# Kernel optimization log

Hardware: AMD Instinct MI355X
Metric: run time of the kernel (lower is better)

Reference implementation:

```python
import jax, jax.numpy as jnp
import numpy as np

N = 16384
E = 262144
HID = 128
NFILT = 128
NGAUSS = 50
NINTER = 6
CUTOFF = 10.0
NUMZ = 100
LOG2 = 0.6931471805599453


def ssp(x):
    # ShiftedSoftplus
    return jax.nn.softplus(x) - LOG2


def setup_inputs() -> dict:
    key = jax.random.key(0)
    ks = jax.random.split(key, 20)
    z = jax.random.randint(ks[0], (N,), 0, NUMZ)
    pos = jax.random.uniform(ks[1], (N, 3), dtype=jnp.float32) * 5.0  # box side 5 -> all pairs < cutoff
    edge_index = jax.random.randint(ks[2], (2, E), 0, N)
    s = lambda k, shape, fan: jax.random.normal(k, shape, dtype=jnp.float32) / np.sqrt(fan)
    params = dict(
        emb=s(ks[3], (NUMZ, HID), 1.0),
        Wf1=s(ks[4], (NINTER, NGAUSS, NFILT), NGAUSS), bf1=jnp.zeros((NINTER, NFILT), jnp.float32),
        Wf2=s(ks[5], (NINTER, NFILT, NFILT), NFILT), bf2=jnp.zeros((NINTER, NFILT), jnp.float32),
        Wl1=s(ks[6], (NINTER, HID, NFILT), HID),
        Wl2=s(ks[7], (NINTER, NFILT, HID), NFILT), bl2=jnp.zeros((NINTER, HID), jnp.float32),
        Wl=s(ks[8], (NINTER, HID, HID), HID), bl=jnp.zeros((NINTER, HID), jnp.float32),
        Wo1=s(ks[9], (HID, HID // 2), HID), bo1=jnp.zeros((HID // 2,), jnp.float32),
        Wo2=s(ks[10], (HID // 2, 1), HID // 2), bo2=jnp.zeros((1,), jnp.float32),
    )
    return dict(z=z, pos=pos, edge_index=edge_index, **params)


def reference(z, pos, edge_index, emb, Wf1, bf1, Wf2, bf2, Wl1, Wl2, bl2, Wl, bl, Wo1, bo1, Wo2, bo2):
    src, dst = edge_index[0], edge_index[1]
    # edge distances and Gaussian smearing
    d = jnp.linalg.norm(pos[src] - pos[dst], axis=-1)          # [E]
    offset = jnp.linspace(0.0, CUTOFF, NGAUSS, dtype=jnp.float32)
    coeff = -0.5 / (offset[1] - offset[0]) ** 2
    ea = jnp.exp(coeff * (d[:, None] - offset) ** 2)            # [E, NGAUSS]
    C = 0.5 * (jnp.cos(d * (np.pi / CUTOFF)) + 1.0)             # cosine cutoff [E]

    h = emb[z]                                                  # [N, HID]
    for i in range(NINTER):
        # continuous-filter weights
        Wfilt = (ssp(ea @ Wf1[i] + bf1[i]) @ Wf2[i] + bf2[i]) * C[:, None]  # [E, NFILT]
        x = h @ Wl1[i]                                          # lin1, no bias [N, NFILT]
        msg = x[src] * Wfilt                                    # gather + filter
        agg = jax.ops.segment_sum(msg, dst, num_segments=N)     # scatter-sum [N, NFILT]
        x = ssp(agg @ Wl2[i] + bl2[i]) @ Wl[i] + bl[i]          # lin2 -> ssp -> lin
        h = h + x

    h = ssp(h @ Wo1 + bo1) @ Wo2 + bo2                          # [N, 1] per-atom energy
    out = jnp.sum(h, axis=0, keepdims=True)                     # 'add' readout, single graph -> [1, 1]
    return jax.nn.relu(out)
```

## Files before the change

kernel.cpp:

```cpp
#include <hip/hip_runtime.h>
#include <math.h>

#define NATOM 16384
#define NEDGE 262144
#define HID 128
#define NG 50
#define NI 6

typedef _Float16 h8_t __attribute__((ext_vector_type(8)));
typedef _Float16 h4_t __attribute__((ext_vector_type(4)));
typedef float    f4_t __attribute__((ext_vector_type(4)));

__device__ __forceinline__ float ssp_f(float v) {
    float e = __expf(-fabsf(v));
    return fmaxf(v, 0.0f) + __logf(1.0f + e) - 0.69314718055994531f;
}

__global__ void fill0(float* __restrict__ p, int n4) {
    int i = blockIdx.x * 256 + threadIdx.x;
    if (i < n4) ((float4*)p)[i] = make_float4(0.f, 0.f, 0.f, 0.f);
}

__global__ void hist_k(const int* __restrict__ ei, int* __restrict__ cnt) {
    int e = blockIdx.x * 256 + threadIdx.x;
    if (e < NEDGE) atomicAdd(&cnt[ei[NEDGE + e]], 1);
}

__global__ void scan_k(const int* __restrict__ cnt, int* __restrict__ offs) {
    __shared__ int part[256];
    int t = threadIdx.x;
    int base = t * 64;
    int s = 0;
    for (int i = 0; i < 64; ++i) s += cnt[base + i];
    part[t] = s;
    __syncthreads();
    for (int off = 1; off < 256; off <<= 1) {
        int v = (t >= off) ? part[t - off] : 0;
        __syncthreads();
        part[t] += v;
        __syncthreads();
    }
    int r = part[t] - s;
    for (int i = 0; i < 64; ++i) { offs[base + i] = r; r += cnt[base + i]; }
    if (t == 255) offs[NATOM] = r;
}

__global__ void scatter_k(const int* __restrict__ ei, const int* __restrict__ offs,
                          int* __restrict__ cnt, int* __restrict__ sSrc, int* __restrict__ sDst) {
    int e = blockIdx.x * 256 + threadIdx.x;
    if (e >= NEDGE) return;
    int d = ei[NEDGE + e];
    int r = atomicAdd(&cnt[d], 1);
    int j = offs[d] + r;
    sSrc[j] = ei[e];
    sDst[j] = d;
}

__global__ void edge_pre(const float* __restrict__ pos,
                         const int* __restrict__ sSrc, const int* __restrict__ sDst,
                         _Float16* __restrict__ ea, float* __restrict__ Cb) {
    int j = blockIdx.x * 256 + threadIdx.x;
    if (j >= NEDGE) return;
    int s = sSrc[j], dd = sDst[j];
    float dx = pos[3*s]   - pos[3*dd];
    float dy = pos[3*s+1] - pos[3*dd+1];
    float dz = pos[3*s+2] - pos[3*dd+2];
    float d = sqrtf(dx*dx + dy*dy + dz*dz);
    Cb[j] = 0.5f * (cosf(d * 0.31415926535897931f) + 1.0f);
    const float delta = 10.0f / 49.0f;
    const float coeff = -0.5f / (delta * delta);
    #pragma unroll
    for (int gq = 0; gq < 8; ++gq) {
        h8_t hv;
        #pragma unroll
        for (int r = 0; r < 8; ++r) {
            int g = gq * 8 + r;
            float v = 0.0f;
            if (g < NG) { float u = d - (float)g * delta; v = __expf(coeff * u * u); }
            hv[r] = (_Float16)v;
        }
        *(h8_t*)&ea[(size_t)j * 64 + gq * 8] = hv;
    }
}

__global__ void wprep(const float* __restrict__ Wf1, const float* __restrict__ Wf2,
                      const float* __restrict__ Wl1, const float* __restrict__ Wl2,
                      const float* __restrict__ Wl,
                      _Float16* __restrict__ w1, _Float16* __restrict__ w2,
                      _Float16* __restrict__ wnh, _Float16* __restrict__ wnl) {
    int idx = blockIdx.x * 256 + threadIdx.x;
    const int S1 = NI * 128 * 64, S2 = NI * 128 * 128;
    if (idx < S1) {
        int i = idx >> 13, r = idx & 8191, fo = r >> 6, k = r & 63;
        float v = (k < NG) ? Wf1[(size_t)i * NG * 128 + k * 128 + fo] : 0.0f;
        w1[idx] = (_Float16)v;
        return;
    }
    idx -= S1;
    if (idx < S2) {
        int i = idx >> 14, r = idx & 16383, fo = r >> 7, k = r & 127;
        w2[idx] = (_Float16)Wf2[(size_t)i * 128 * 128 + k * 128 + fo];
        return;
    }
    idx -= S2;
    if (idx < 3 * S2) {
        int mi = idx >> 14;
        int r = idx & 16383, fo = r >> 7, k = r & 127;
        int m = mi / NI, i = mi % NI;
        const float* W = (m == 0) ? Wl1 : (m == 1) ? Wl2 : Wl;
        float v = W[(size_t)i * 128 * 128 + k * 128 + fo];
        _Float16 hh = (_Float16)v;
        wnh[idx] = hh; wnl[idx] = (_Float16)(v - (float)hh);
    }
}

__global__ void embed_k(const int* __restrict__ z, const float* __restrict__ emb,
                        float* __restrict__ h) {
    int tid = blockIdx.x * 256 + threadIdx.x;
    int n = tid >> 7, f = tid & 127;
    h[tid] = emb[z[n] * HID + f];
}

__launch_bounds__(256)
__global__ void gemm_node_mfma(const float* __restrict__ A,
                               const _Float16* __restrict__ wth, const _Float16* __restrict__ wtl,
                               _Float16* __restrict__ xh) {
    __shared__ _Float16 aH[64 * 136];
    __shared__ _Float16 aL[64 * 136];
    int t = threadIdx.x;
    int mb = blockIdx.x * 64;
    #pragma unroll
    for (int j = 0; j < 8; ++j) {
        int idx = t + j * 256;
        int row = idx >> 5, c4 = idx & 31;
        f4_t v = *(const f4_t*)&A[(size_t)(mb + row) * HID + c4 * 4];
        h4_t hh, ll;
        #pragma unroll
        for (int r = 0; r < 4; ++r) {
            _Float16 hx = (_Float16)v[r];
            hh[r] = hx; ll[r] = (_Float16)(v[r] - (float)hx);
        }
        *(h4_t*)&aH[row * 136 + c4 * 4] = hh;
        *(h4_t*)&aL[row * 136 + c4 * 4] = ll;
    }
    __syncthreads();

    int wv = t >> 6, lane = t & 63, l15 = lane & 15, quad = lane >> 4;
    f4_t acc[2][4];
    #pragma unroll
    for (int m = 0; m < 2; ++m)
        #pragma unroll
        for (int n = 0; n < 4; ++n) acc[m][n] = (f4_t)0.0f;

    for (int kc = 0; kc < 4; ++kc) {
        int k0 = kc * 32 + quad * 8;
        h8_t a_h[2], a_l[2];
        #pragma unroll
        for (int m = 0; m < 2; ++m) {
            int fr = wv * 32 + m * 16 + l15;
            a_h[m] = *(const h8_t*)&wth[fr * 128 + k0];
            a_l[m] = *(const h8_t*)&wtl[fr * 128 + k0];
        }
        #pragma unroll
        for (int n = 0; n < 4; ++n) {
            int er = n * 16 + l15;
            h8_t b_h = *(const h8_t*)&aH[er * 136 + k0];
            h8_t b_l = *(const h8_t*)&aL[er * 136 + k0];
            #pragma unroll
            for (int m = 0; m < 2; ++m) {
                acc[m][n] = __builtin_amdgcn_mfma_f32_16x16x32_f16(a_h[m], b_h, acc[m][n], 0, 0, 0);
                acc[m][n] = __builtin_amdgcn_mfma_f32_16x16x32_f16(a_h[m], b_l, acc[m][n], 0, 0, 0);
                acc[m][n] = __builtin_amdgcn_mfma_f32_16x16x32_f16(a_l[m], b_h, acc[m][n], 0, 0, 0);
            }
        }
    }

    #pragma unroll
    for (int n = 0; n < 4; ++n) {
        int el = n * 16 + l15;
        size_t row = (size_t)(mb + el);
        #pragma unroll
        for (int m = 0; m < 2; ++m) {
            int fb = wv * 32 + m * 16 + quad * 4;
            h4_t o;
            #pragma unroll
            for (int r = 0; r < 4; ++r) o[r] = (_Float16)acc[m][n][r];
            *(h4_t*)&xh[row * 128 + fb] = o;
        }
    }
}

__launch_bounds__(256)
__global__ void gemm_node3(const float* __restrict__ agg,
                           const _Float16* __restrict__ w2th, const _Float16* __restrict__ w2tl,
                           const _Float16* __restrict__ wlth, const _Float16* __restrict__ wltl,
                           const _Float16* __restrict__ w1nh, const _Float16* __restrict__ w1nl,
                           const float* __restrict__ bl2, const float* __restrict__ bl,
                           float* __restrict__ h, _Float16* __restrict__ xh) {
    __shared__ _Float16 aH[64 * 136];
    __shared__ _Float16 aL[64 * 136];
    int t = threadIdx.x;
    int mb = blockIdx.x * 64;
    #pragma unroll
    for (int j = 0; j < 8; ++j) {
        int idx = t + j * 256;
        int row = idx >> 5, c4 = idx & 31;
        f4_t v = *(const f4_t*)&agg[(size_t)(mb + row) * HID + c4 * 4];
        h4_t hh, ll;
        #pragma unroll
        for (int r = 0; r < 4; ++r) {
            _Float16 hx = (_Float16)v[r];
            hh[r] = hx; ll[r] = (_Float16)(v[r] - (float)hx);
        }
        *(h4_t*)&aH[row * 136 + c4 * 4] = hh;
        *(h4_t*)&aL[row * 136 + c4 * 4] = ll;
    }
    __syncthreads();

    int wv = t >> 6, lane = t & 63, l15 = lane & 15, quad = lane >> 4;
    int fq = wv * 32 + quad * 4;
    f4_t acc[2][4];

    #pragma unroll
    for (int m = 0; m < 2; ++m)
        #pragma unroll
        for (int n = 0; n < 4; ++n) acc[m][n] = (f4_t)0.0f;
    for (int kc = 0; kc < 4; ++kc) {
        int k0 = kc * 32 + quad * 8;
        h8_t a_h[2], a_l[2];
        #pragma unroll
        for (int m = 0; m < 2; ++m) {
            int fr = wv * 32 + m * 16 + l15;
            a_h[m] = *(const h8_t*)&w2th[fr * 128 + k0];
            a_l[m] = *(const h8_t*)&w2tl[fr * 128 + k0];
        }
        #pragma unroll
        for (int n = 0; n < 4; ++n) {
            int er = n * 16 + l15;
            h8_t b_h = *(const h8_t*)&aH[er * 136 + k0];
            h8_t b_l = *(const h8_t*)&aL[er * 136 + k0];
            #pragma unroll
            for (int m = 0; m < 2; ++m) {
                acc[m][n] = __builtin_amdgcn_mfma_f32_16x16x32_f16(a_h[m], b_h, acc[m][n], 0, 0, 0);
                acc[m][n] = __builtin_amdgcn_mfma_f32_16x16x32_f16(a_h[m], b_l, acc[m][n], 0, 0, 0);
                acc[m][n] = __builtin_amdgcn_mfma_f32_16x16x32_f16(a_l[m], b_h, acc[m][n], 0, 0, 0);
            }
        }
    }
    f4_t b2v[2];
    b2v[0] = *(const f4_t*)&bl2[fq]; b2v[1] = *(const f4_t*)&bl2[fq + 16];
    __syncthreads();

    #pragma unroll
    for (int m = 0; m < 2; ++m)
        #pragma unroll
        for (int n = 0; n < 4; ++n) {
            int el = n * 16 + l15;
            int fb = wv * 32 + m * 16 + quad * 4;
            h4_t hh, ll;
            #pragma unroll
            for (int r = 0; r < 4; ++r) {
                float sv = ssp_f(acc[m][n][r] + b2v[m][r]);
                _Float16 hx = (_Float16)sv;
                hh[r] = hx;
                ll[r] = (_Float16)(sv - (float)hx);
            }
            *(h4_t*)&aH[el * 136 + fb] = hh;
            *(h4_t*)&aL[el * 136 + fb] = ll;
        }
    __syncthreads();

    #pragma unroll
    for (int m = 0; m < 2; ++m)
        #pragma unroll
        for (int n = 0; n < 4; ++n) acc[m][n] = (f4_t)0.0f;
    for (int kc = 0; kc < 4; ++kc) {
        int k0 = kc * 32 + quad * 8;
        h8_t a_h[2], a_l[2];
        #pragma unroll
        for (int m = 0; m < 2; ++m) {
            int fr = wv * 32 + m * 16 + l15;
            a_h[m] = *(const h8_t*)&wlth[fr * 128 + k0];
            a_l[m] = *(const h8_t*)&wltl[fr * 128 + k0];
        }
        #pragma unroll
        for (int n = 0; n < 4; ++n) {
            int er = n * 16 + l15;
            h8_t b_h = *(const h8_t*)&aH[er * 136 + k0];
            h8_t b_l = *(const h8_t*)&aL[er * 136 + k0];
            #pragma unroll
            for (int m = 0; m < 2; ++m) {
                acc[m][n] = __builtin_amdgcn_mfma_f32_16x16x32_f16(a_h[m], b_h, acc[m][n], 0, 0, 0);
                acc[m][n] = __builtin_amdgcn_mfma_f32_16x16x32_f16(a_h[m], b_l, acc[m][n], 0, 0, 0);
                acc[m][n] = __builtin_amdgcn_mfma_f32_16x16x32_f16(a_l[m], b_h, acc[m][n], 0, 0, 0);
            }
        }
    }
    f4_t blv[2];
    blv[0] = *(const f4_t*)&bl[fq]; blv[1] = *(const f4_t*)&bl[fq + 16];
    __syncthreads();

    #pragma unroll
    for (int n = 0; n < 4; ++n) {
        int el = n * 16 + l15;
        size_t row = (size_t)(mb + el);
        #pragma unroll
        for (int m = 0; m < 2; ++m) {
            int fb = wv * 32 + m * 16 + quad * 4;
            f4_t hv = *(const f4_t*)&h[row * 128 + fb];
            f4_t o;
            h4_t hh, ll;
            #pragma unroll
            for (int r = 0; r < 4; ++r) {
                o[r] = hv[r] + acc[m][n][r] + blv[m][r];
                _Float16 hx = (_Float16)o[r];
                hh[r] = hx; ll[r] = (_Float16)(o[r] - (float)hx);
            }
            *(f4_t*)&h[row * 128 + fb] = o;
            *(h4_t*)&aH[el * 136 + fb] = hh;
            *(h4_t*)&aL[el * 136 + fb] = ll;
        }
    }
    if (!w1nh) return;
    __syncthreads();

    #pragma unroll
    for (int m = 0; m < 2; ++m)
        #pragma unroll
        for (int n = 0; n < 4; ++n) acc[m][n] = (f4_t)0.0f;
    for (int kc = 0; kc < 4; ++kc) {
        int k0 = kc * 32 + quad * 8;
        h8_t a_h[2], a_l[2];
        #pragma unroll
        for (int m = 0; m < 2; ++m) {
            int fr = wv * 32 + m * 16 + l15;
            a_h[m] = *(const h8_t*)&w1nh[fr * 128 + k0];
            a_l[m] = *(const h8_t*)&w1nl[fr * 128 + k0];
        }
        #pragma unroll
        for (int n = 0; n < 4; ++n) {
            int er = n * 16 + l15;
            h8_t b_h = *(const h8_t*)&aH[er * 136 + k0];
            h8_t b_l = *(const h8_t*)&aL[er * 136 + k0];
            #pragma unroll
            for (int m = 0; m < 2; ++m) {
                acc[m][n] = __builtin_amdgcn_mfma_f32_16x16x32_f16(a_h[m], b_h, acc[m][n], 0, 0, 0);
                acc[m][n] = __builtin_amdgcn_mfma_f32_16x16x32_f16(a_h[m], b_l, acc[m][n], 0, 0, 0);
                acc[m][n] = __builtin_amdgcn_mfma_f32_16x16x32_f16(a_l[m], b_h, acc[m][n], 0, 0, 0);
            }
        }
    }
    #pragma unroll
    for (int n = 0; n < 4; ++n) {
        int el = n * 16 + l15;
        size_t row = (size_t)(mb + el);
        #pragma unroll
        for (int m = 0; m < 2; ++m) {
            int fb = wv * 32 + m * 16 + quad * 4;
            h4_t o;
            #pragma unroll
            for (int r = 0; r < 4; ++r) o[r] = (_Float16)acc[m][n][r];
            *(h4_t*)&xh[row * 128 + fb] = o;
        }
    }
}

#define T1_LDW 136
#define EA_LDW 72
#define EF_TPB 4

__launch_bounds__(256, 4)
__global__ void edge_filter(const _Float16* __restrict__ xh, float* __restrict__ agg,
                            const int* __restrict__ sSrc, const int* __restrict__ sDst,
                            const float* __restrict__ Cb,
                            const _Float16* __restrict__ ea,
                            const _Float16* __restrict__ w1, const _Float16* __restrict__ w2,
                            const float* __restrict__ bf1, const float* __restrict__ bf2) {
    __shared__ __align__(16) _Float16 eaS[64 * EA_LDW];
    __shared__ __align__(16) _Float16 t1S[64 * T1_LDW];
    __shared__ int dstl[64];

    _Float16* msg = t1S;

    int t = threadIdx.x;
    int wv = t >> 6, lane = t & 63;
    int l15 = lane & 15, quad = lane >> 4;
    int tile0 = blockIdx.x * EF_TPB;

    h8_t w1f[2][2], w2f[4][2];
    #pragma unroll
    for (int kc = 0; kc < 2; ++kc) {
        int k0 = kc * 32 + quad * 8;
        #pragma unroll
        for (int m = 0; m < 2; ++m)
            w1f[kc][m] = *(const h8_t*)&w1[(wv * 32 + m * 16 + l15) * 64 + k0];
    }
    #pragma unroll
    for (int kc = 0; kc < 4; ++kc) {
        int k0 = kc * 32 + quad * 8;
        #pragma unroll
        for (int m = 0; m < 2; ++m)
            w2f[kc][m] = *(const h8_t*)&w2[(wv * 32 + m * 16 + l15) * 128 + k0];
    }
    int fq = wv * 32 + quad * 4;
    f4_t b1v[2], b2v[2];
    b1v[0] = *(const f4_t*)&bf1[fq];  b1v[1] = *(const f4_t*)&bf1[fq + 16];
    b2v[0] = *(const f4_t*)&bf2[fq];  b2v[1] = *(const f4_t*)&bf2[fq + 16];

    int srcn[4], dstn[4];
    float cn[4];
    {
        int eb = tile0 * 64;
        #pragma unroll
        for (int n = 0; n < 4; ++n) {
            int ge = eb + n * 16 + l15;
            srcn[n] = sSrc[ge];
            dstn[n] = sDst[ge];
            cn[n]   = Cb[ge];
        }
        if (t < 64) dstl[t] = sDst[eb + t];
        #pragma unroll
        for (int c = 0; c < 2; ++c) {
            int ch = t + c * 256;
            int e = ch >> 3, ks = ch & 7;
            *(h8_t*)&eaS[e * EA_LDW + ks * 8] = *(const h8_t*)&ea[(size_t)(eb + e) * 64 + ks * 8];
        }
    }
    __syncthreads();

    for (int tt = 0; tt < EF_TPB; ++tt) {
        bool pre = (tt < EF_TPB - 1);
        h8_t sreg[2];
        int srcp[4], dstp[4];
        float cp[4];
        if (pre) {
            int ebn = (tile0 + tt + 1) * 64;
            #pragma unroll
            for (int c = 0; c < 2; ++c) {
                int ch = t + c * 256;
                int e = ch >> 3, ks = ch & 7;
                sreg[c] = *(const h8_t*)&ea[(size_t)(ebn + e) * 64 + ks * 8];
            }
            #pragma unroll
            for (int n = 0; n < 4; ++n) {
                int ge = ebn + n * 16 + l15;
                srcp[n] = sSrc[ge];
                dstp[n] = sDst[ge];
                cp[n]   = Cb[ge];
            }
        }
        h4_t xr[4][2];
        #pragma unroll
        for (int n = 0; n < 4; ++n)
            #pragma unroll
            for (int m = 0; m < 2; ++m)
                xr[n][m] = *(const h4_t*)&xh[(size_t)srcn[n] * HID + wv * 32 + m * 16 + quad * 4];

        f4_t acc1[2][4];
        #pragma unroll
        for (int m = 0; m < 2; ++m)
            #pragma unroll
            for (int n = 0; n < 4; ++n) acc1[m][n] = (f4_t)0.0f;
        #pragma unroll
        for (int kc = 0; kc < 2; ++kc) {
            int k0 = kc * 32 + quad * 8;
            h8_t b[4];
            #pragma unroll
            for (int n = 0; n < 4; ++n)
                b[n] = *(const h8_t*)&eaS[(n * 16 + l15) * EA_LDW + k0];
            #pragma unroll
            for (int m = 0; m < 2; ++m)
                #pragma unroll
                for (int n = 0; n < 4; ++n)
                    acc1[m][n] = __builtin_amdgcn_mfma_f32_16x16x32_f16(w1f[kc][m], b[n], acc1[m][n], 0, 0, 0);
        }

        #pragma unroll
        for (int m = 0; m < 2; ++m)
            #pragma unroll
            for (int n = 0; n < 4; ++n) {
                int el = n * 16 + l15;
                int fb = wv * 32 + m * 16 + quad * 4;
                h4_t hh;
                #pragma unroll
                for (int r = 0; r < 4; ++r)
                    hh[r] = (_Float16)ssp_f(acc1[m][n][r] + b1v[m][r]);
                *(h4_t*)&t1S[el * T1_LDW + fb] = hh;
            }
        __syncthreads();

        if (pre) {
            #pragma unroll
            for (int c = 0; c < 2; ++c) {
                int ch = t + c * 256;
                int e = ch >> 3, ks = ch & 7;
                *(h8_t*)&eaS[e * EA_LDW + ks * 8] = sreg[c];
            }
        }

        f4_t acc2[2][4];
        #pragma unroll
        for (int m = 0; m < 2; ++m)
            #pragma unroll
            for (int n = 0; n < 4; ++n) acc2[m][n] = (f4_t)0.0f;
        #pragma unroll
        for (int kc = 0; kc < 4; ++kc) {
            int k0 = kc * 32 + quad * 8;
            #pragma unroll
            for (int n = 0; n < 4; ++n) {
                h8_t b = *(const h8_t*)&t1S[(n * 16 + l15) * T1_LDW + k0];
                #pragma unroll
                for (int m = 0; m < 2; ++m)
                    acc2[m][n] = __builtin_amdgcn_mfma_f32_16x16x32_f16(w2f[kc][m], b, acc2[m][n], 0, 0, 0);
            }
        }
        __syncthreads();

        #pragma unroll
        for (int n = 0; n < 4; ++n) {
            int el = n * 16 + l15;
            float ce = cn[n];
            #pragma unroll
            for (int m = 0; m < 2; ++m) {
                int fb = wv * 32 + m * 16 + quad * 4;
                h4_t o;
                #pragma unroll
                for (int r = 0; r < 4; ++r)
                    o[r] = (_Float16)((acc2[m][n][r] + b2v[m][r]) * ce * (float)xr[n][m][r]);
                *(h4_t*)&msg[el * T1_LDW + fb] = o;
            }
        }
        __syncthreads();

        {
            int f = t & 127, hf = t >> 7;
            int ib = hf * 32;
            float run = 0.0f;
            int cur = dstl[ib];
            for (int i = ib; i < ib + 32; ++i) {
                int dnow = dstl[i];
                if (dnow != cur) {
                    atomicAdd(&agg[(size_t)cur * HID + f], run);
                    run = 0.0f;
                    cur = dnow;
                }
                run += (float)msg[i * T1_LDW + f];
            }
            atomicAdd(&agg[(size_t)cur * HID + f], run);
        }

        if (pre) {
            #pragma unroll
            for (int n = 0; n < 4; ++n) { srcn[n] = srcp[n]; dstn[n] = dstp[n]; cn[n] = cp[n]; }
            __syncthreads();
            if (t < 64) dstl[t] = dstp[t >> 4] ;
        }
    }
}

__launch_bounds__(256)
__global__ void readout1(const float* __restrict__ h, const float* __restrict__ Wo1,
                         const float* __restrict__ bo1, const float* __restrict__ Wo2,
                         const float* __restrict__ bo2, float* __restrict__ accum) {
    __shared__ float w1[128 * 64];
    __shared__ float part[4];
    int t = threadIdx.x;
    for (int i = t; i < 128 * 16; i += 256)
        ((float4*)w1)[i] = ((const float4*)Wo1)[i];
    __syncthreads();
    int f = t & 63, wv = t >> 6;
    float b = bo1[f], w2v = Wo2[f];
    float lsum = 0.0f;
    for (int a = 0; a < 16; ++a) {
        int n = blockIdx.x * 64 + wv * 16 + a;
        const float* hr = &h[(size_t)n * HID];
        float acc = b;
        #pragma unroll 16
        for (int k = 0; k < 128; ++k)
            acc = fmaf(hr[k], w1[k*64 + f], acc);
        lsum += ssp_f(acc) * w2v;
    }
    #pragma unroll
    for (int off = 32; off > 0; off >>= 1)
        lsum += __shfl_down(lsum, off, 64);
    if (f == 0) part[wv] = lsum;
    __syncthreads();
    if (t == 0)
        atomicAdd(accum, part[0] + part[1] + part[2] + part[3] + 64.0f * bo2[0]);
}

__global__ void readout2(const float* __restrict__ accum, float* __restrict__ out) {
    out[0] = fmaxf(accum[0], 0.0f);
}

extern "C" void kernel_launch(void* const* d_in, const int* in_sizes, int n_in,
                              void* d_out, int out_size, void* d_ws, size_t ws_size,
                              hipStream_t stream) {
    const int*   z   = (const int*)d_in[0];
    const float* pos = (const float*)d_in[1];
    const int*   ei  = (const int*)d_in[2];
    const float* emb = (const float*)d_in[3];
    const float* Wf1 = (const float*)d_in[4];
    const float* bf1 = (const float*)d_in[5];
    const float* Wf2 = (const float*)d_in[6];
    const float* bf2 = (const float*)d_in[7];
    const float* Wl1 = (const float*)d_in[8];
    const float* Wl2 = (const float*)d_in[9];
    const float* bl2 = (const float*)d_in[10];
    const float* Wl  = (const float*)d_in[11];
    const float* bl  = (const float*)d_in[12];
    const float* Wo1 = (const float*)d_in[13];
    const float* bo1 = (const float*)d_in[14];
    const float* Wo2 = (const float*)d_in[15];
    const float* bo2 = (const float*)d_in[16];
    float* out = (float*)d_out;

    _Float16* w1  = (_Float16*)d_ws;
    _Float16* w2  = w1 + NI * 8192;
    _Float16* wnh = w2 + NI * 16384;
    _Float16* wnl = wnh + 3 * NI * 16384;
    _Float16* ea  = wnl + 3 * NI * 16384;
    _Float16* xh  = ea + (size_t)NEDGE * 64;
    float* Cb  = (float*)(xh + (size_t)NATOM * 128);
    float* h   = Cb + NEDGE;
    float* agg = h + (size_t)NATOM * HID;
    float* accum = agg + (size_t)NATOM * HID;
    int* cnt  = (int*)(accum + 4);
    int* offs = cnt + NATOM;
    int* sSrc = offs + NATOM + 4;
    int* sDst = sSrc + NEDGE;

    fill0<<<NATOM/4/256, 256, 0, stream>>>((float*)cnt, NATOM/4);
    hist_k<<<NEDGE/256, 256, 0, stream>>>(ei, cnt);
    scan_k<<<1, 256, 0, stream>>>(cnt, offs);
    fill0<<<NATOM/4/256, 256, 0, stream>>>((float*)cnt, NATOM/4);
    scatter_k<<<NEDGE/256, 256, 0, stream>>>(ei, offs, cnt, sSrc, sDst);

    edge_pre<<<NEDGE/256, 256, 0, stream>>>(pos, sSrc, sDst, ea, Cb);
    wprep<<<(NI*8192 + NI*16384 + 3*NI*16384)/256, 256, 0, stream>>>(
        Wf1, Wf2, Wl1, Wl2, Wl, w1, w2, wnh, wnl);
    embed_k<<<(NATOM*HID)/256, 256, 0, stream>>>(z, emb, h);

    gemm_node_mfma<<<256, 256, 0, stream>>>(h, wnh + (size_t)0*16384,
        wnl + (size_t)0*16384, xh);
    for (int i = 0; i < NI; ++i) {
        fill0<<<(NATOM*HID/4)/256, 256, 0, stream>>>(agg, NATOM*HID/4);
        edge_filter<<<NEDGE/64/EF_TPB, 256, 0, stream>>>(xh, agg, sSrc, sDst, Cb, ea,
            w1 + (size_t)i*8192, w2 + (size_t)i*16384,
            bf1 + i*HID, bf2 + i*HID);
        const _Float16* w1nh = (i < NI-1) ? wnh + (size_t)(i+1)*16384 : nullptr;
        const _Float16* w1nl = (i < NI-1) ? wnl + (size_t)(i+1)*16384 : nullptr;
        gemm_node3<<<256, 256, 0, stream>>>(agg,
            wnh + (size_t)(1*NI+i)*16384, wnl + (size_t)(1*NI+i)*16384,
            wnh + (size_t)(2*NI+i)*16384, wnl + (size_t)(2*NI+i)*16384,
            w1nh, w1nl, bl2 + i*HID, bl + i*HID, h, xh);
    }
    fill0<<<1, 256, 0, stream>>>(accum, 1);
    readout1<<<NATOM/64, 256, 0, stream>>>(h, Wo1, bo1, Wo2, bo2, accum);
    readout2<<<1, 1, 0, stream>>>(accum, out);
}
```

Before: 807.4 us.

## Partition edge filter by destination-node ranges and accumulate in shared memory

Each block now owns 16 consecutive destination nodes and walks their CSR-sorted edge range. Messages are reduced into a shared-memory accumulator, and each block writes its slice of agg once. This removes the per-layer zero-fill of agg and the global atomics. It also drops the software prefetch of the next tile, adds a barrier per tile, and makes the per-block work depend on the degree distribution, which can leave tail tiles partly empty.

```diff
diff --git a/kernel.cpp b/kernel.cpp
--- a/kernel.cpp
+++ b/kernel.cpp
@@ -367,17 +367,18 @@
 
 #define T1_LDW 136
 #define EA_LDW 72
-#define EF_TPB 4
+#define NDST 16
 
 __launch_bounds__(256, 4)
 __global__ void edge_filter(const _Float16* __restrict__ xh, float* __restrict__ agg,
                             const int* __restrict__ sSrc, const int* __restrict__ sDst,
-                            const float* __restrict__ Cb,
+                            const int* __restrict__ offs, const float* __restrict__ Cb,
                             const _Float16* __restrict__ ea,
                             const _Float16* __restrict__ w1, const _Float16* __restrict__ w2,
                             const float* __restrict__ bf1, const float* __restrict__ bf2) {
     __shared__ __align__(16) _Float16 eaS[64 * EA_LDW];
     __shared__ __align__(16) _Float16 t1S[64 * T1_LDW];
+    __shared__ float accS[NDST * 128];
     __shared__ int dstl[64];
 
     _Float16* msg = t1S;
@@ -385,7 +386,14 @@
     int t = threadIdx.x;
     int wv = t >> 6, lane = t & 63;
     int l15 = lane & 15, quad = lane >> 4;
-    int tile0 = blockIdx.x * EF_TPB;
+    int d0 = blockIdx.x * NDST;
+    int estart = offs[d0];
+    int ecnt = offs[d0 + NDST] - estart;
+    int tmax = (ecnt + 63) >> 6;
+
+    #pragma unroll
+    for (int c = 0; c < 2; ++c)
+        *(f4_t*)&accS[(t + c * 256) * 4] = (f4_t)0.0f;
 
     h8_t w1f[2][2], w2f[4][2];
     #pragma unroll
@@ -407,47 +415,31 @@
     b1v[0] = *(const f4_t*)&bf1[fq];  b1v[1] = *(const f4_t*)&bf1[fq + 16];
     b2v[0] = *(const f4_t*)&bf2[fq];  b2v[1] = *(const f4_t*)&bf2[fq + 16];
 
-    int srcn[4], dstn[4];
-    float cn[4];
-    {
-        int eb = tile0 * 64;
-        #pragma unroll
-        for (int n = 0; n < 4; ++n) {
-            int ge = eb + n * 16 + l15;
-            srcn[n] = sSrc[ge];
-            dstn[n] = sDst[ge];
-            cn[n]   = Cb[ge];
-        }
-        if (t < 64) dstl[t] = sDst[eb + t];
+    for (int tt = 0; tt < tmax; ++tt) {
+        int base = estart + tt * 64;
+        int lim = ecnt - tt * 64;
+
         #pragma unroll
         for (int c = 0; c < 2; ++c) {
             int ch = t + c * 256;
             int e = ch >> 3, ks = ch & 7;
-            *(h8_t*)&eaS[e * EA_LDW + ks * 8] = *(const h8_t*)&ea[(size_t)(eb + e) * 64 + ks * 8];
-        }
-    }
-    __syncthreads();
-
-    for (int tt = 0; tt < EF_TPB; ++tt) {
-        bool pre = (tt < EF_TPB - 1);
-        h8_t sreg[2];
-        int srcp[4], dstp[4];
-        float cp[4];
-        if (pre) {
-            int ebn = (tile0 + tt + 1) * 64;
-            #pragma unroll
-            for (int c = 0; c < 2; ++c) {
-                int ch = t + c * 256;
-                int e = ch >> 3, ks = ch & 7;
-                sreg[c] = *(const h8_t*)&ea[(size_t)(ebn + e) * 64 + ks * 8];
-            }
-            #pragma unroll
-            for (int n = 0; n < 4; ++n) {
-                int ge = ebn + n * 16 + l15;
-                srcp[n] = sSrc[ge];
-                dstp[n] = sDst[ge];
-                cp[n]   = Cb[ge];
-            }
+            h8_t v = (h8_t)(_Float16)0.0f;
+            if (e < lim) v = *(const h8_t*)&ea[(size_t)(base + e) * 64 + ks * 8];
+            *(h8_t*)&eaS[e * EA_LDW + ks * 8] = v;
+        }
+        if (t < 64) {
+            int dl = 0;
+            if (t < lim) dl = sDst[base + t] - d0;
+            dstl[t] = dl;
+        }
+        int srcn[4];
+        float cn[4];
+        #pragma unroll
+        for (int n = 0; n < 4; ++n) {
+            int rel = n * 16 + l15;
+            bool ok = rel < lim;
+            srcn[n] = ok ? sSrc[base + rel] : 0;
+            cn[n]   = ok ? Cb[base + rel] : 0.0f;
         }
         h4_t xr[4][2];
         #pragma unroll
@@ -455,6 +447,7 @@
             #pragma unroll
             for (int m = 0; m < 2; ++m)
                 xr[n][m] = *(const h4_t*)&xh[(size_t)srcn[n] * HID + wv * 32 + m * 16 + quad * 4];
+        __syncthreads();
 
         f4_t acc1[2][4];
         #pragma unroll
@@ -489,15 +482,6 @@
             }
         __syncthreads();
 
-        if (pre) {
-            #pragma unroll
-            for (int c = 0; c < 2; ++c) {
-                int ch = t + c * 256;
-                int e = ch >> 3, ks = ch & 7;
-                *(h8_t*)&eaS[e * EA_LDW + ks * 8] = sreg[c];
-            }
-        }
-
         f4_t acc2[2][4];
         #pragma unroll
         for (int m = 0; m < 2; ++m)
@@ -540,21 +524,22 @@
             for (int i = ib; i < ib + 32; ++i) {
                 int dnow = dstl[i];
                 if (dnow != cur) {
-                    atomicAdd(&agg[(size_t)cur * HID + f], run);
+                    atomicAdd(&accS[cur * 128 + f], run);
                     run = 0.0f;
                     cur = dnow;
                 }
                 run += (float)msg[i * T1_LDW + f];
             }
-            atomicAdd(&agg[(size_t)cur * HID + f], run);
-        }
-
-        if (pre) {
-            #pragma unroll
-            for (int n = 0; n < 4; ++n) { srcn[n] = srcp[n]; dstn[n] = dstp[n]; cn[n] = cp[n]; }
-            __syncthreads();
-            if (t < 64) dstl[t] = dstp[t >> 4] ;
-        }
+            atomicAdd(&accS[cur * 128 + f], run);
+        }
+        __syncthreads();
+    }
+
+    float* dstp = &agg[(size_t)d0 * HID];
+    #pragma unroll
+    for (int c = 0; c < 2; ++c) {
+        int idx = t + c * 256;
+        *(f4_t*)&dstp[idx * 4] = *(const f4_t*)&accS[idx * 4];
     }
 }
 
@@ -644,8 +629,7 @@
     gemm_node_mfma<<<256, 256, 0, stream>>>(h, wnh + (size_t)0*16384,
         wnl + (size_t)0*16384, xh);
     for (int i = 0; i < NI; ++i) {
-        fill0<<<(NATOM*HID/4)/256, 256, 0, stream>>>(agg, NATOM*HID/4);
-        edge_filter<<<NEDGE/64/EF_TPB, 256, 0, stream>>>(xh, agg, sSrc, sDst, Cb, ea,
+        edge_filter<<<NATOM/NDST, 256, 0, stream>>>(xh, agg, sSrc, sDst, offs, Cb, ea,
             w1 + (size_t)i*8192, w2 + (size_t)i*16384,
             bf1 + i*HID, bf2 + i*HID);
         const _Float16* w1nh = (i < NI-1) ? wnh + (size_t)(i+1)*16384 : nullptr;
```

New measurement: 784.3 us. 1.03x faster.
